# Kernel tuning notes

Hardware: AMD Instinct MI355X
Metric: run time of the kernel (lower is better)

Reference implementation:

```python
import jax, jax.numpy as jnp
import numpy as np

B, S, D, N, L, V = 2, 512, 1024, 4096, 4, 32000
EPS = 1e-5

def ternarize(w):
    # BitNet b1.58-style: scale = mean |w|, quantize to {-1,0,1}, rescale.
    s = jnp.mean(jnp.abs(w)) + 1e-8
    return s * jnp.round(jnp.clip(w / s, -1.0, 1.0))

def tern_ste(w):
    # straight-through estimator (faithful to ternary training)
    return w + jax.lax.stop_gradient(ternarize(w) - w)

def layer_norm(x, g, b):
    mu = jnp.mean(x, axis=-1, keepdims=True)
    var = jnp.var(x, axis=-1, keepdims=True)
    return (x - mu) * jax.lax.rsqrt(var + EPS) * g + b

def setup_inputs() -> dict:
    key = jax.random.key(0)
    ks = jax.random.split(key, 20)
    sc = lambda d: 1.0 / np.sqrt(d)
    inp = {
        'input_ids': jax.random.randint(ks[0], (B, S), 0, V, dtype=jnp.int32),
        'emb':       jax.random.normal(ks[1], (V, D), jnp.float32) * 0.02,
        'pos_emb':   jax.random.normal(ks[2], (S, D), jnp.float32) * 0.02,
        'gru_wih':   jax.random.normal(ks[3], (3 * D, D), jnp.float32) * sc(D),
        'gru_whh':   jax.random.normal(ks[4], (3 * D, D), jnp.float32) * sc(D),
        'gru_bih':   jnp.zeros((3 * D,), jnp.float32),
        'gru_bhh':   jnp.zeros((3 * D,), jnp.float32),
        'syn_w':     jax.random.normal(ks[5], (L, N, D), jnp.float32) * sc(D),
        'syn_b':     jnp.zeros((L, N), jnp.float32),
        'out_w':     jax.random.normal(ks[6], (L, D, N), jnp.float32) * sc(N),
        'out_b':     jnp.zeros((L, D), jnp.float32),
        'ln_g':      jnp.ones((L, D), jnp.float32),
        'ln_b':      jnp.zeros((L, D), jnp.float32),
        'on_g':      jnp.ones((D,), jnp.float32),
        'on_b':      jnp.zeros((D,), jnp.float32),
        'head_w':    jax.random.normal(ks[7], (V, D), jnp.float32) * sc(D),
        'head_b':    jnp.zeros((V,), jnp.float32),
    }
    return inp

def gru(x, wih, whh, bih, bhh):
    # x: [B,S,D] -> [B,S,D], torch nn.GRU semantics, h0 = 0
    # Precompute input projections for all timesteps: [B,S,3D]
    gi_all = jnp.einsum('bsd,ed->bse', x, wih) + bih
    def step(h, gi):
        gh = h @ whh.T + bhh
        ir, iz, inn = jnp.split(gi, 3, axis=-1)
        hr, hz, hn = jnp.split(gh, 3, axis=-1)
        r = jax.nn.sigmoid(ir + hr)
        z = jax.nn.sigmoid(iz + hz)
        n = jnp.tanh(inn + r * hn)
        h_new = (1.0 - z) * n + z * h
        return h_new, h_new
    h0 = jnp.zeros((x.shape[0], whh.shape[1]), x.dtype)
    _, hs = jax.lax.scan(step, h0, jnp.swapaxes(gi_all, 0, 1))
    return jnp.swapaxes(hs, 0, 1)

def reference(input_ids, emb, pos_emb, gru_wih, gru_whh, gru_bih, gru_bhh,
              syn_w, syn_b, out_w, out_b, ln_g, ln_b, on_g, on_b,
              head_w, head_b):
    # Ternary embedding lookup
    x = tern_ste(emb)[input_ids]                       # [B,S,D]
    x = x + pos_emb[None, :x.shape[1], :]
    x = gru(x, gru_wih, gru_whh, gru_bih, gru_bhh)
    for l in range(L):
        residual = x
        hidden = jax.nn.relu(jnp.einsum('bsd,nd->bsn', x, tern_ste(syn_w[l])) + syn_b[l])
        out = jnp.einsum('bsn,dn->bsd', hidden, tern_ste(out_w[l])) + out_b[l]
        x = layer_norm(residual + out, ln_g[l], ln_b[l])
    x = layer_norm(x, on_g, on_b)
    logits = jnp.einsum('bsd,vd->bsv', x, tern_ste(head_w)) + head_b  # [B,S,V]
    return logits
```

## Files before the change

### kernel.cpp

```cpp
#include <hip/hip_runtime.h>
#include <hip/hip_bf16.h>
#include <cstdint>
#include <cstddef>

#define Dm 1024
#define Sm 512
#define Bm 2
#define Nm 4096
#define Lm 4
#define Vm 32000

typedef __attribute__((ext_vector_type(8))) short short8;
typedef __attribute__((ext_vector_type(4))) float floatx4;

struct PrepArgs {
  const float* src[9];
  unsigned short* dst[9];
  long n4[9];
  int sidx[9];
  int njobs;
};

__device__ __forceinline__ unsigned short f2b(float f){
  union { float f; unsigned u; } v; v.f = f;
  unsigned r = (v.u + 0x7fffu + ((v.u >> 16) & 1u)) >> 16;
  return (unsigned short)r;
}
__device__ __forceinline__ float b2f(unsigned short h){
  union { unsigned u; float f; } v; v.u = ((unsigned)h) << 16;
  return v.f;
}

__device__ __forceinline__ void gload16(const unsigned short* g, unsigned short* l){
  __builtin_amdgcn_global_load_lds(
      (const __attribute__((address_space(1))) void*)g,
      (__attribute__((address_space(3))) void*)l, 16, 0, 0);
}

__global__ __launch_bounds__(256) void absum_all_kernel(
    const float* __restrict__ emb, const float* __restrict__ syn_w,
    const float* __restrict__ out_w, const float* __restrict__ head_w,
    double* __restrict__ partial)
{
  int wid = blockIdx.x >> 7;
  int blk = blockIdx.x & 127;
  const float* base; long n4;
  if (wid == 0){ base = emb; n4 = (long)Vm * Dm / 4; }
  else if (wid <= 4){ base = syn_w + (size_t)(wid - 1) * Nm * Dm; n4 = (long)Nm * Dm / 4; }
  else if (wid <= 8){ base = out_w + (size_t)(wid - 5) * Dm * Nm; n4 = (long)Nm * Dm / 4; }
  else { base = head_w; n4 = (long)Vm * Dm / 4; }

  long i = (long)blk * 256 + threadIdx.x;
  const long stride = 128L * 256;
  double s = 0.0;
  for (; i < n4; i += stride){
    float4 v = ((const float4*)base)[i];
    s += (double)fabsf(v.x) + (double)fabsf(v.y) + (double)fabsf(v.z) + (double)fabsf(v.w);
  }
  #pragma unroll
  for (int off = 32; off; off >>= 1) s += __shfl_down(s, off, 64);
  __shared__ double wsum[4];
  int lane = threadIdx.x & 63, wv = threadIdx.x >> 6;
  if (lane == 0) wsum[wv] = s;
  __syncthreads();
  if (threadIdx.x == 0) partial[wid * 128 + blk] = wsum[0] + wsum[1] + wsum[2] + wsum[3];
}

__global__ __launch_bounds__(128) void scale_kernel(const double* __restrict__ partials,
                                                    float* __restrict__ scales){
  int b = blockIdx.x;
  int tid = threadIdx.x;
  __shared__ double red[128];
  red[tid] = partials[b * 128 + tid];
  __syncthreads();
  for (int off = 64; off; off >>= 1){
    if (tid < off) red[tid] += red[tid + off];
    __syncthreads();
  }
  if (tid == 0){
    double cnt = (b == 0 || b == 9) ? (double)Vm * (double)Dm : (double)Nm * (double)Dm;
    scales[b] = (float)(red[0] / cnt);
  }
}

__global__ __launch_bounds__(256) void tern_kernel(const float* __restrict__ w,
                                                   const float* __restrict__ smean,
                                                   unsigned short* __restrict__ out, long n4){
  float s = smean[0] + 1e-8f;
  long i = (long)blockIdx.x * blockDim.x + threadIdx.x;
  long stride = (long)gridDim.x * blockDim.x;
  for (; i < n4; i += stride){
    float4 v = ((const float4*)w)[i];
    ushort4 o;
    o.x = f2b(rintf(fminf(fmaxf(v.x / s, -1.f), 1.f)));
    o.y = f2b(rintf(fminf(fmaxf(v.y / s, -1.f), 1.f)));
    o.z = f2b(rintf(fminf(fmaxf(v.z / s, -1.f), 1.f)));
    o.w = f2b(rintf(fminf(fmaxf(v.w / s, -1.f), 1.f)));
    ((ushort4*)out)[i] = o;
  }
}

__global__ __launch_bounds__(256) void embed_split_kernel(
    const int* __restrict__ ids, const float* __restrict__ emb,
    const float* __restrict__ pos, const float* __restrict__ smean,
    unsigned short* __restrict__ xhi, unsigned short* __restrict__ xlo,
    const float* __restrict__ wih, unsigned short* __restrict__ whi,
    unsigned short* __restrict__ wlo)
{
  if (blockIdx.x < 1024){
    int row = blockIdx.x;
    int sp  = row & (Sm - 1);
    int id  = ids[row];
    float s = smean[0] + 1e-8f;
    int d = threadIdx.x * 4;
    float4 wv = *(const float4*)(emb + (size_t)id * Dm + d);
    float4 pv = *(const float4*)(pos + (size_t)sp * Dm + d);
    float y[4];
    y[0] = s * rintf(fminf(fmaxf(wv.x / s, -1.f), 1.f)) + pv.x;
    y[1] = s * rintf(fminf(fmaxf(wv.y / s, -1.f), 1.f)) + pv.y;
    y[2] = s * rintf(fminf(fmaxf(wv.z / s, -1.f), 1.f)) + pv.z;
    y[3] = s * rintf(fminf(fmaxf(wv.w / s, -1.f), 1.f)) + pv.w;
    ushort4 h4, l4;
    unsigned short* hp = (unsigned short*)&h4;
    unsigned short* lp = (unsigned short*)&l4;
    #pragma unroll
    for (int e = 0; e < 4; e++){
      unsigned short h = f2b(y[e]);
      hp[e] = h;
      lp[e] = f2b(y[e] - b2f(h));
    }
    size_t base = (size_t)row * Dm + d;
    *(ushort4*)(xhi + base) = h4;
    *(ushort4*)(xlo + base) = l4;
  } else {
    long i = (long)(blockIdx.x - 1024) * 256 + threadIdx.x;
    const long stride = 1024L * 256;
    const long n4 = (long)(3 * Dm) * Dm / 4;
    for (; i < n4; i += stride){
      float4 v = ((const float4*)wih)[i];
      float f[4] = {v.x, v.y, v.z, v.w};
      ushort4 h4, l4;
      unsigned short* hp = (unsigned short*)&h4;
      unsigned short* lp = (unsigned short*)&l4;
      #pragma unroll
      for (int e = 0; e < 4; e++){
        unsigned short h = f2b(f[e]);
        hp[e] = h;
        lp[e] = f2b(f[e] - b2f(h));
      }
      ((ushort4*)whi)[i] = h4;
      ((ushort4*)wlo)[i] = l4;
    }
  }
}

template<bool WSPLIT, bool WF32, int BT>
__global__ __launch_bounds__(256) void gemm_kernel(
    const unsigned short* __restrict__ Ahi, const unsigned short* __restrict__ Alo,
    const void* __restrict__ Wsrc, const unsigned short* __restrict__ Wlo,
    const float* __restrict__ bias, const float* __restrict__ smean,
    int relu, float* __restrict__ outf,
    unsigned short* __restrict__ outhi, unsigned short* __restrict__ outlo,
    int M, int N, int K)
{
  constexpr int WT = BT / 2;
  constexpr int FT = WT / 16;
  constexpr int RPT = 256 / BT;
  constexpr int CPT = 32 / RPT;
  constexpr int NU  = CPT / 8;

  __shared__ unsigned short As[2][BT][40];
  __shared__ unsigned short Bs[WSPLIT ? 2 : 1][BT][40];
  int tid = threadIdx.x;
  int wave = tid >> 6, lane = tid & 63;
  int wm = wave >> 1, wn = wave & 1;
  int bm = blockIdx.y, bn = blockIdx.x;

  bool tern = (smean != nullptr);
  float s = 1.f;
  if (tern) s = smean[0] + 1e-8f;

  int arow = tid / RPT, sub = tid % RPT;
  int col0 = sub * CPT;
  const unsigned short* Agh = Ahi + (size_t)(bm * BT + arow) * K + col0;
  const unsigned short* Agl = Alo + (size_t)(bm * BT + arow) * K + col0;
  const float* Wgf = nullptr;
  const unsigned short* Wgh = nullptr;
  const unsigned short* Wgl = nullptr;
  if (WF32) Wgf = (const float*)Wsrc + (size_t)(bn * BT + arow) * K + col0;
  else {
    Wgh = (const unsigned short*)Wsrc + (size_t)(bn * BT + arow) * K + col0;
    if (WSPLIT) Wgl = Wlo + (size_t)(bn * BT + arow) * K + col0;
  }

  floatx4 acc[FT][FT];
  #pragma unroll
  for (int i = 0; i < FT; i++)
    #pragma unroll
    for (int j = 0; j < FT; j++)
      acc[i][j] = (floatx4){0.f, 0.f, 0.f, 0.f};

  int kpb = K / (int)gridDim.z;
  int k_beg = blockIdx.z * kpb;

  for (int k0 = k_beg; k0 < k_beg + kpb; k0 += 32){
    __syncthreads();
    #pragma unroll
    for (int u = 0; u < NU; u++){
      *(uint4*)&As[0][arow][col0 + u * 8] = *(const uint4*)(Agh + k0 + u * 8);
      *(uint4*)&As[1][arow][col0 + u * 8] = *(const uint4*)(Agl + k0 + u * 8);
    }
    if (WF32){
      unsigned short tmp[CPT];
      #pragma unroll
      for (int q = 0; q < CPT / 4; q++){
        float4 wv = *(const float4*)(Wgf + k0 + q * 4);
        float f[4] = {wv.x, wv.y, wv.z, wv.w};
        #pragma unroll
        for (int e = 0; e < 4; e++){
          float w = f[e];
          if (tern) w = rintf(fminf(fmaxf(w / s, -1.f), 1.f));
          tmp[q * 4 + e] = f2b(w);
        }
      }
      #pragma unroll
      for (int u = 0; u < NU; u++)
        *(uint4*)&Bs[0][arow][col0 + u * 8] = *(uint4*)&tmp[u * 8];
    } else {
      #pragma unroll
      for (int u = 0; u < NU; u++){
        *(uint4*)&Bs[0][arow][col0 + u * 8] = *(const uint4*)(Wgh + k0 + u * 8);
        if (WSPLIT)
          *(uint4*)&Bs[1][arow][col0 + u * 8] = *(const uint4*)(Wgl + k0 + u * 8);
      }
    }
    __syncthreads();

    int kq = lane >> 4, mr = lane & 15;
    short8 afh[FT], afl[FT], bfh[FT];
    #pragma unroll
    for (int i = 0; i < FT; i++){
      afh[i] = *(const short8*)&As[0][wm*WT + i*16 + mr][kq*8];
      afl[i] = *(const short8*)&As[1][wm*WT + i*16 + mr][kq*8];
    }
    #pragma unroll
    for (int j = 0; j < FT; j++) bfh[j] = *(const short8*)&Bs[0][wn*WT + j*16 + mr][kq*8];
    #pragma unroll
    for (int i = 0; i < FT; i++)
      #pragma unroll
      for (int j = 0; j < FT; j++){
        acc[i][j] = __builtin_amdgcn_mfma_f32_16x16x32_bf16(afh[i], bfh[j], acc[i][j], 0, 0, 0);
        acc[i][j] = __builtin_amdgcn_mfma_f32_16x16x32_bf16(afl[i], bfh[j], acc[i][j], 0, 0, 0);
      }
    if (WSPLIT){
      short8 bfl[FT];
      #pragma unroll
      for (int j = 0; j < FT; j++) bfl[j] = *(const short8*)&Bs[1][wn*WT + j*16 + mr][kq*8];
      #pragma unroll
      for (int i = 0; i < FT; i++)
        #pragma unroll
        for (int j = 0; j < FT; j++)
          acc[i][j] = __builtin_amdgcn_mfma_f32_16x16x32_bf16(afh[i], bfl[j], acc[i][j], 0, 0, 0);
    }
  }

  bool split = (gridDim.z > 1);
  bool addb = (blockIdx.z == 0);
  int cr = lane >> 4, cc = lane & 15;
  #pragma unroll
  for (int j = 0; j < FT; j++){
    int col = bn * BT + wn * WT + j * 16 + cc;
    float bv = (bias && addb) ? bias[col] : 0.f;
    #pragma unroll
    for (int i = 0; i < FT; i++){
      #pragma unroll
      for (int r = 0; r < 4; r++){
        int row = bm * BT + wm * WT + i * 16 + cr * 4 + r;
        float v = acc[i][j][r] * s + bv;
        if (relu) v = fmaxf(v, 0.f);
        size_t idx = (size_t)row * N + col;
        if (outf){
          if (split) atomicAdd(outf + idx, v);
          else outf[idx] = v;
        }
        if (outhi){
          unsigned short h = f2b(v);
          outhi[idx] = h;
          outlo[idx] = f2b(v - b2f(h));
        }
      }
    }
  }
}

__global__ __launch_bounds__(256) void gemm_lds_kernel(
    const unsigned short* __restrict__ Ahi, const unsigned short* __restrict__ Alo,
    const unsigned short* __restrict__ Whi,
    const float* __restrict__ bias, const float* __restrict__ smean,
    int relu, float* __restrict__ outf, int M, int N, int K)
{
  int nbm = M / 128, nbn = N / 128;
  int id = blockIdx.x;
  int xcd = id & 7;
  int sblk = id >> 3;
  int bm = sblk % nbm;
  int q = sblk / nbm;
  int bn = xcd + 8 * q;
  if (bn >= nbn) return;

  __shared__ __align__(16) unsigned short lds[3 * 4096];
  int tid = threadIdx.x;
  int wave = tid >> 6, lane = tid & 63;
  int wm = wave >> 1, wn = wave & 1;

  float s = 1.f;
  if (smean) s = smean[0] + 1e-8f;

  int r0 = wave * 32 + (lane >> 2);
  int r1 = r0 + 16;
  int s0 = (lane & 3) ^ ((r0 >> 1) & 3);
  int s1 = (lane & 3) ^ ((r1 >> 1) & 3);
  const unsigned short* ga0 = Ahi + (size_t)(bm * 128 + r0) * K + s0 * 8;
  const unsigned short* ga1 = Ahi + (size_t)(bm * 128 + r1) * K + s1 * 8;
  const unsigned short* gl0 = Alo + (size_t)(bm * 128 + r0) * K + s0 * 8;
  const unsigned short* gl1 = Alo + (size_t)(bm * 128 + r1) * K + s1 * 8;
  const unsigned short* gw0 = Whi + (size_t)(bn * 128 + r0) * K + s0 * 8;
  const unsigned short* gw1 = Whi + (size_t)(bn * 128 + r1) * K + s1 * 8;
  unsigned short* la = &lds[wave * 1024];

  floatx4 acc[4][4];
  #pragma unroll
  for (int i = 0; i < 4; i++)
    #pragma unroll
    for (int j = 0; j < 4; j++)
      acc[i][j] = (floatx4){0.f, 0.f, 0.f, 0.f};

  for (int k0 = 0; k0 < K; k0 += 32){
    __syncthreads();
    gload16(ga0 + k0, la);
    gload16(ga1 + k0, la + 512);
    gload16(gl0 + k0, la + 4096);
    gload16(gl1 + k0, la + 4096 + 512);
    gload16(gw0 + k0, la + 8192);
    gload16(gw1 + k0, la + 8192 + 512);
    __syncthreads();

    int kq = lane >> 4, mr = lane & 15;
    short8 afh[4], afl[4], bfh[4];
    #pragma unroll
    for (int i = 0; i < 4; i++){
      int r = wm * 64 + i * 16 + mr;
      int off = r * 32 + ((kq ^ ((r >> 1) & 3)) << 3);
      afh[i] = *(const short8*)&lds[off];
      afl[i] = *(const short8*)&lds[4096 + off];
    }
    #pragma unroll
    for (int j = 0; j < 4; j++){
      int r = wn * 64 + j * 16 + mr;
      int off = r * 32 + ((kq ^ ((r >> 1) & 3)) << 3);
      bfh[j] = *(const short8*)&lds[8192 + off];
    }
    #pragma unroll
    for (int i = 0; i < 4; i++)
      #pragma unroll
      for (int j = 0; j < 4; j++){
        acc[i][j] = __builtin_amdgcn_mfma_f32_16x16x32_bf16(afh[i], bfh[j], acc[i][j], 0, 0, 0);
        acc[i][j] = __builtin_amdgcn_mfma_f32_16x16x32_bf16(afl[i], bfh[j], acc[i][j], 0, 0, 0);
      }
  }

  int cr = lane >> 4, cc = lane & 15;
  #pragma unroll
  for (int j = 0; j < 4; j++){
    int col = bn * 128 + wn * 64 + j * 16 + cc;
    float bv = bias ? bias[col] : 0.f;
    #pragma unroll
    for (int i = 0; i < 4; i++){
      #pragma unroll
      for (int r = 0; r < 4; r++){
        int row = bm * 128 + wm * 64 + i * 16 + cr * 4 + r;
        float v = acc[i][j][r] * s + bv;
        if (relu) v = fmaxf(v, 0.f);
        outf[(size_t)row * N + col] = v;
      }
    }
  }
}

#define NGRU 64
__global__ __launch_bounds__(1024) void gru_kernel(
    const float* __restrict__ gi, const float* __restrict__ whh, const float* __restrict__ bhh,
    unsigned long long* __restrict__ hbuf, float* __restrict__ hs,
    unsigned short* __restrict__ xhi, unsigned short* __restrict__ xlo,
    const float* __restrict__ scales, PrepArgs pa)
{
  if (blockIdx.x >= NGRU){
    long pid = blockIdx.x - NGRU;
    long stride = (long)(gridDim.x - NGRU) * 1024;
    for (int j = 0; j < pa.njobs; j++){
      float s = scales[pa.sidx[j]] + 1e-8f;
      const float4* s4 = (const float4*)pa.src[j];
      ushort4* d4 = (ushort4*)pa.dst[j];
      long n4 = pa.n4[j];
      for (long k = pid * 1024 + threadIdx.x; k < n4; k += stride){
        float4 v = s4[k];
        ushort4 o;
        o.x = f2b(rintf(fminf(fmaxf(v.x / s, -1.f), 1.f)));
        o.y = f2b(rintf(fminf(fmaxf(v.y / s, -1.f), 1.f)));
        o.z = f2b(rintf(fminf(fmaxf(v.z / s, -1.f), 1.f)));
        o.w = f2b(rintf(fminf(fmaxf(v.w / s, -1.f), 1.f)));
        d4[k] = o;
      }
    }
    return;
  }

  __shared__ float lds_h[2 * 1088];
  __shared__ float lds_gh[96];
  int w = blockIdx.x, tid = threadIdx.x;
  int d0 = w * 16;
  int o = tid >> 4, c = tid & 15;
  bool active = (o < 48);
  int g = o >> 4, dl = o & 15;
  int wrow = g * Dm + d0 + dl;
  float wreg[64];
  if (active){
    const float* src = whh + (size_t)wrow * Dm + c * 64;
    #pragma unroll
    for (int i = 0; i < 64; i++) wreg[i] = src[i];
  }
  float bhval = active ? bhh[wrow] : 0.f;

  int bb = tid >> 4, dd = tid & 15;
  float hprev = 0.f;

  for (int t = 0; t < Sm; t++){
    float ir = 0.f, iz = 0.f, inn = 0.f;
    if (tid < 32){
      const float* girow = gi + ((size_t)bb * Sm + t) * (3 * Dm);
      int d = d0 + dd;
      ir  = girow[d];
      iz  = girow[Dm + d];
      inn = girow[2 * Dm + d];
    }
    {
      const unsigned long long* src = hbuf + (size_t)(t & 1) * 2048 + tid * 2;
      unsigned got = 0;
      int spins = 0;
      while (got != 3u){
        #pragma unroll
        for (int q = 0; q < 2; q++){
          if (!(got & (1u << q))){
            unsigned long long wd = __hip_atomic_load(src + q, __ATOMIC_RELAXED,
                                                      __HIP_MEMORY_SCOPE_AGENT);
            if ((unsigned)(wd >> 32) == (unsigned)t){
              union { unsigned u; float f; } cv; cv.u = (unsigned)wd;
              int wi = tid * 2 + q;
              int b = wi >> 10, d = wi & 1023;
              lds_h[b * 1088 + (d >> 6) * 68 + (d & 63)] = cv.f;
              got |= 1u << q;
            }
          }
        }
        if (got != 3u){
          if (++spins > (1 << 20)) break;
          __builtin_amdgcn_s_sleep(1);
        }
      }
    }
    __syncthreads();
    if (active){
      const float* hp = lds_h + c * 68;
      float a0 = 0.f, a1 = 0.f;
      #pragma unroll
      for (int q = 0; q < 16; q++){
        float4 h0 = *(const float4*)(hp + q * 4);
        float4 h1 = *(const float4*)(hp + 1088 + q * 4);
        a0 += wreg[q*4+0] * h0.x; a1 += wreg[q*4+0] * h1.x;
        a0 += wreg[q*4+1] * h0.y; a1 += wreg[q*4+1] * h1.y;
        a0 += wreg[q*4+2] * h0.z; a1 += wreg[q*4+2] * h1.z;
        a0 += wreg[q*4+3] * h0.w; a1 += wreg[q*4+3] * h1.w;
      }
      #pragma unroll
      for (int off = 8; off; off >>= 1){
        a0 += __shfl_xor(a0, off, 16);
        a1 += __shfl_xor(a1, off, 16);
      }
      if (c == 0){
        lds_gh[o]      = a0 + bhval;
        lds_gh[48 + o] = a1 + bhval;
      }
    }
    __syncthreads();
    if (tid < 32){
      float gr = lds_gh[bb * 48 + dd];
      float gz = lds_gh[bb * 48 + 16 + dd];
      float gn = lds_gh[bb * 48 + 32 + dd];
      float rr = 1.f / (1.f + expf(-(ir + gr)));
      float zz = 1.f / (1.f + expf(-(iz + gz)));
      float nn = tanhf(inn + rr * gn);
      float hnew = (1.f - zz) * nn + zz * hprev;
      hprev = hnew;
      int d = d0 + dd;
      union { float f; unsigned u; } cv; cv.f = hnew;
      unsigned long long wd = ((unsigned long long)(unsigned)(t + 1) << 32) | (unsigned long long)cv.u;
      __hip_atomic_store(hbuf + (size_t)((t + 1) & 1) * 2048 + bb * Dm + d, wd,
                         __ATOMIC_RELAXED, __HIP_MEMORY_SCOPE_AGENT);
      size_t oi = ((size_t)bb * Sm + t) * Dm + d;
      hs[oi] = hnew;
      unsigned short h = f2b(hnew);
      xhi[oi] = h;
      xlo[oi] = f2b(hnew - b2f(h));
    }
  }
}

__global__ __launch_bounds__(256) void ln_kernel(
    const float* __restrict__ resid, const float* __restrict__ addv,
    const float* __restrict__ g, const float* __restrict__ b,
    float* __restrict__ outf, unsigned short* __restrict__ outhi,
    unsigned short* __restrict__ outlo)
{
  int row = blockIdx.x;
  int d = threadIdx.x * 4;
  size_t base = (size_t)row * Dm + d;
  float4 v = *(const float4*)(resid + base);
  if (addv){
    float4 a = *(const float4*)(addv + base);
    v.x += a.x; v.y += a.y; v.z += a.z; v.w += a.w;
  }
  float sum = v.x + v.y + v.z + v.w;
  float sq  = v.x*v.x + v.y*v.y + v.z*v.z + v.w*v.w;
  #pragma unroll
  for (int off = 32; off; off >>= 1){
    sum += __shfl_down(sum, off, 64);
    sq  += __shfl_down(sq,  off, 64);
  }
  __shared__ float red[4][2];
  __shared__ float bc[2];
  int lane = threadIdx.x & 63, wv = threadIdx.x >> 6;
  if (lane == 0){ red[wv][0] = sum; red[wv][1] = sq; }
  __syncthreads();
  if (threadIdx.x == 0){
    float st = red[0][0] + red[1][0] + red[2][0] + red[3][0];
    float qt = red[0][1] + red[1][1] + red[2][1] + red[3][1];
    float mu = st * (1.f / Dm);
    float var = qt * (1.f / Dm) - mu * mu;
    bc[0] = mu; bc[1] = rsqrtf(var + 1e-5f);
  }
  __syncthreads();
  float mu = bc[0], rs = bc[1];
  float4 gv = *(const float4*)(g + d);
  float4 bv = *(const float4*)(b + d);
  float y[4];
  y[0] = (v.x - mu) * rs * gv.x + bv.x;
  y[1] = (v.y - mu) * rs * gv.y + bv.y;
  y[2] = (v.z - mu) * rs * gv.z + bv.z;
  y[3] = (v.w - mu) * rs * gv.w + bv.w;
  if (outf) *(float4*)(outf + base) = *(float4*)y;
  if (outhi){
    ushort4 h4, l4;
    unsigned short* hp = (unsigned short*)&h4;
    unsigned short* lp = (unsigned short*)&l4;
    #pragma unroll
    for (int e = 0; e < 4; e++){
      unsigned short h = f2b(y[e]);
      hp[e] = h;
      lp[e] = f2b(y[e] - b2f(h));
    }
    *(ushort4*)(outhi + base) = h4;
    *(ushort4*)(outlo + base) = l4;
  }
}

extern "C" void kernel_launch(void* const* d_in, const int* in_sizes, int n_in,
                              void* d_out, int out_size, void* d_ws, size_t ws_size,
                              hipStream_t stream)
{
  const int*   ids    = (const int*)  d_in[0];
  const float* emb    = (const float*)d_in[1];
  const float* pos    = (const float*)d_in[2];
  const float* wih    = (const float*)d_in[3];
  const float* whh    = (const float*)d_in[4];
  const float* bih    = (const float*)d_in[5];
  const float* bhh    = (const float*)d_in[6];
  const float* syn_w  = (const float*)d_in[7];
  const float* syn_b  = (const float*)d_in[8];
  const float* out_w  = (const float*)d_in[9];
  const float* out_b  = (const float*)d_in[10];
  const float* ln_g   = (const float*)d_in[11];
  const float* ln_b   = (const float*)d_in[12];
  const float* on_g   = (const float*)d_in[13];
  const float* on_b   = (const float*)d_in[14];
  const float* head_w = (const float*)d_in[15];
  const float* head_b = (const float*)d_in[16];
  float* logits = (float*)d_out;

  const size_t MB = (size_t)1 << 20;
  char* ws = (char*)d_ws;
  float*  scales   = (float*) ws;
  double* partials = (double*)(ws + 32768);
  unsigned long long* hbuf = (unsigned long long*)(ws + 131072);
  float*          hs     = (float*)         (ws + 1  * MB);
  unsigned short* xhi    = (unsigned short*)(ws + 5  * MB);
  unsigned short* xlo    = (unsigned short*)(ws + 7  * MB);
  float*          outbuf = (float*)         (ws + 9  * MB);
  float*          gi     = (float*)         (ws + 13 * MB);
  unsigned short* ltbuf  = (unsigned short*)(ws + 13 * MB);
  unsigned short* wih_hi = (unsigned short*)(ws + 25 * MB);
  unsigned short* wih_lo = (unsigned short*)(ws + 31 * MB);
  unsigned short* hhi    = (unsigned short*)(ws + 37 * MB);
  unsigned short* hlo    = (unsigned short*)(ws + 45 * MB);
  unsigned short* wbuf   = (unsigned short*)(ws + 53 * MB);

  bool pre_layer = ws_size >= 62  * MB;
  bool pre_head  = ws_size >= 120 * MB;
  bool tier1     = ws_size >= 192 * MB;

  PrepArgs pa; pa.njobs = 0;
  unsigned short* synp[Lm] = {nullptr, nullptr, nullptr, nullptr};
  unsigned short* outp[Lm] = {nullptr, nullptr, nullptr, nullptr};
  auto addjob = [&](const float* s, unsigned short* d, long n4, int si){
    pa.src[pa.njobs] = s; pa.dst[pa.njobs] = d; pa.n4[pa.njobs] = n4; pa.sidx[pa.njobs] = si;
    pa.njobs++;
  };
  if (pre_head){
    addjob(head_w, wbuf, (long)Vm * Dm / 4, 9);
    if (tier1){
      for (int l = 0; l < Lm; l++){
        synp[l] = (unsigned short*)(ws + 120 * MB + (size_t)l * 8 * MB);
        outp[l] = (unsigned short*)(ws + 152 * MB + (size_t)l * 8 * MB);
        addjob(syn_w + (size_t)l * Nm * Dm, synp[l], (long)Nm * Dm / 4, 1 + l);
        addjob(out_w + (size_t)l * Dm * Nm, outp[l], (long)Nm * Dm / 4, 5 + l);
      }
    } else {
      synp[0] = (unsigned short*)(ws + 25 * MB);
      addjob(syn_w, synp[0], (long)Nm * Dm / 4, 1);
    }
  }

  hipMemsetAsync(d_ws, 0, 163840, stream);

  absum_all_kernel<<<1280, 256, 0, stream>>>(emb, syn_w, out_w, head_w, partials);
  scale_kernel<<<10, 128, 0, stream>>>(partials, scales);

  embed_split_kernel<<<2048, 256, 0, stream>>>(ids, emb, pos, scales, xhi, xlo,
                                               wih, wih_hi, wih_lo);

  gemm_kernel<true, false, 64><<<dim3(3072/64, 1024/64, 1), 256, 0, stream>>>(
      xhi, xlo, wih_hi, wih_lo, bih, nullptr, 0, gi, nullptr, nullptr, 1024, 3072, 1024);

  gru_kernel<<<NGRU + 192, 1024, 0, stream>>>(gi, whh, bhh, hbuf, hs, xhi, xlo, scales, pa);

  for (int l = 0; l < Lm; l++){
    if (pre_head){
      unsigned short* sw = synp[l];
      if (!sw){
        tern_kernel<<<2048, 256, 0, stream>>>(syn_w + (size_t)l * Nm * Dm, scales + 1 + l,
                                              ltbuf, (long)Nm * Dm / 4);
        sw = ltbuf;
      }
      gemm_kernel<false, false, 64><<<dim3(4096/64, 1024/64, 1), 256, 0, stream>>>(
          xhi, xlo, sw, nullptr, syn_b + (size_t)l * Nm, scales + 1 + l,
          1, nullptr, hhi, hlo, 1024, 4096, 1024);
      hipMemsetAsync(outbuf, 0, (size_t)1024 * 1024 * 4, stream);
      unsigned short* ow = outp[l];
      if (!ow){
        tern_kernel<<<2048, 256, 0, stream>>>(out_w + (size_t)l * Dm * Nm, scales + 5 + l,
                                              ltbuf, (long)Dm * Nm / 4);
        ow = ltbuf;
      }
      gemm_kernel<false, false, 64><<<dim3(1024/64, 1024/64, 2), 256, 0, stream>>>(
          hhi, hlo, ow, nullptr, out_b + (size_t)l * Dm, scales + 5 + l,
          0, outbuf, nullptr, nullptr, 1024, 1024, 4096);
    } else if (pre_layer){
      tern_kernel<<<2048, 256, 0, stream>>>(syn_w + (size_t)l * Nm * Dm, scales + 1 + l,
                                            wbuf, (long)Nm * Dm / 4);
      gemm_kernel<false, false, 64><<<dim3(4096/64, 1024/64, 1), 256, 0, stream>>>(
          xhi, xlo, wbuf, nullptr, syn_b + (size_t)l * Nm, scales + 1 + l,
          1, nullptr, hhi, hlo, 1024, 4096, 1024);
      hipMemsetAsync(outbuf, 0, (size_t)1024 * 1024 * 4, stream);
      tern_kernel<<<2048, 256, 0, stream>>>(out_w + (size_t)l * Dm * Nm, scales + 5 + l,
                                            wbuf, (long)Dm * Nm / 4);
      gemm_kernel<false, false, 64><<<dim3(1024/64, 1024/64, 2), 256, 0, stream>>>(
          hhi, hlo, wbuf, nullptr, out_b + (size_t)l * Dm, scales + 5 + l,
          0, outbuf, nullptr, nullptr, 1024, 1024, 4096);
    } else {
      gemm_kernel<false, true, 64><<<dim3(4096/64, 1024/64, 1), 256, 0, stream>>>(
          xhi, xlo, syn_w + (size_t)l * Nm * Dm, nullptr, syn_b + (size_t)l * Nm, scales + 1 + l,
          1, nullptr, hhi, hlo, 1024, 4096, 1024);
      hipMemsetAsync(outbuf, 0, (size_t)1024 * 1024 * 4, stream);
      gemm_kernel<false, true, 64><<<dim3(1024/64, 1024/64, 2), 256, 0, stream>>>(
          hhi, hlo, out_w + (size_t)l * Dm * Nm, nullptr, out_b + (size_t)l * Dm, scales + 5 + l,
          0, outbuf, nullptr, nullptr, 1024, 1024, 4096);
    }
    ln_kernel<<<1024, 256, 0, stream>>>(hs, outbuf, ln_g + (size_t)l * Dm, ln_b + (size_t)l * Dm,
                                        hs, xhi, xlo);
  }
  ln_kernel<<<1024, 256, 0, stream>>>(hs, nullptr, on_g, on_b, nullptr, xhi, xlo);

  if (pre_head){
    gemm_lds_kernel<<<2048, 256, 0, stream>>>(
        xhi, xlo, wbuf, head_b, scales + 9, 0, logits, 1024, 32000, 1024);
  } else {
    gemm_kernel<false, true, 128><<<dim3(32000/128, 1024/128, 1), 256, 0, stream>>>(
        xhi, xlo, head_w, nullptr, head_b, scales + 9, 0, logits, nullptr, nullptr, 1024, 32000, 1024);
  }
}
```

Before: 2.132 ms.

## Fold split-K output zeroing into GRU side blocks and layernorm kernel

Removes the per-layer hipMemsetAsync of the split-K output buffer on the tier1 path. The first buffer is zeroed by the GRU kernel's spare prep blocks, and later buffers are zeroed by extra blocks in the preceding layernorm launch, ping-ponging between two buffers. The prep blocks also sleep briefly before starting, likely to let the GRU blocks get scheduled first. This saves several memset launches at the cost of extra blocks, a sleep delay, and reusing the gi region as a second buffer.

```diff
diff --git a/kernel.cpp b/kernel.cpp
--- a/kernel.cpp
+++ b/kernel.cpp
@@ -14,10 +14,10 @@
 typedef __attribute__((ext_vector_type(4))) float floatx4;
 
 struct PrepArgs {
-  const float* src[9];
-  unsigned short* dst[9];
-  long n4[9];
-  int sidx[9];
+  const float* src[10];
+  unsigned short* dst[10];
+  long n4[10];
+  int sidx[10];
   int njobs;
 };
 
@@ -395,21 +395,30 @@
     const float* __restrict__ scales, PrepArgs pa)
 {
   if (blockIdx.x >= NGRU){
+    if (pa.njobs > 0){
+      for (int i = 0; i < 20; i++) __builtin_amdgcn_s_sleep(127);
+    }
     long pid = blockIdx.x - NGRU;
     long stride = (long)(gridDim.x - NGRU) * 1024;
     for (int j = 0; j < pa.njobs; j++){
-      float s = scales[pa.sidx[j]] + 1e-8f;
       const float4* s4 = (const float4*)pa.src[j];
       ushort4* d4 = (ushort4*)pa.dst[j];
       long n4 = pa.n4[j];
-      for (long k = pid * 1024 + threadIdx.x; k < n4; k += stride){
-        float4 v = s4[k];
-        ushort4 o;
-        o.x = f2b(rintf(fminf(fmaxf(v.x / s, -1.f), 1.f)));
-        o.y = f2b(rintf(fminf(fmaxf(v.y / s, -1.f), 1.f)));
-        o.z = f2b(rintf(fminf(fmaxf(v.z / s, -1.f), 1.f)));
-        o.w = f2b(rintf(fminf(fmaxf(v.w / s, -1.f), 1.f)));
-        d4[k] = o;
+      if (s4){
+        float s = scales[pa.sidx[j]] + 1e-8f;
+        for (long k = pid * 1024 + threadIdx.x; k < n4; k += stride){
+          float4 v = s4[k];
+          ushort4 o;
+          o.x = f2b(rintf(fminf(fmaxf(v.x / s, -1.f), 1.f)));
+          o.y = f2b(rintf(fminf(fmaxf(v.y / s, -1.f), 1.f)));
+          o.z = f2b(rintf(fminf(fmaxf(v.z / s, -1.f), 1.f)));
+          o.w = f2b(rintf(fminf(fmaxf(v.w / s, -1.f), 1.f)));
+          d4[k] = o;
+        }
+      } else {
+        ushort4 z = make_ushort4(0, 0, 0, 0);
+        for (long k = pid * 1024 + threadIdx.x; k < n4; k += stride)
+          d4[k] = z;
       }
     }
     return;
@@ -519,8 +528,18 @@
     const float* __restrict__ resid, const float* __restrict__ addv,
     const float* __restrict__ g, const float* __restrict__ b,
     float* __restrict__ outf, unsigned short* __restrict__ outhi,
-    unsigned short* __restrict__ outlo)
+    unsigned short* __restrict__ outlo, float* __restrict__ zbuf)
 {
+  if (blockIdx.x >= 1024){
+    if (zbuf){
+      long i = (long)(blockIdx.x - 1024) * 256 + threadIdx.x;
+      float4 z = {0.f, 0.f, 0.f, 0.f};
+      #pragma unroll
+      for (int q = 0; q < 4; q++)
+        ((float4*)zbuf)[i + (long)q * 65536] = z;
+    }
+    return;
+  }
   int row = blockIdx.x;
   int d = threadIdx.x * 4;
   size_t base = (size_t)row * Dm + d;
@@ -604,8 +623,9 @@
   float*          hs     = (float*)         (ws + 1  * MB);
   unsigned short* xhi    = (unsigned short*)(ws + 5  * MB);
   unsigned short* xlo    = (unsigned short*)(ws + 7  * MB);
-  float*          outbuf = (float*)         (ws + 9  * MB);
+  float*          outbufA = (float*)        (ws + 9  * MB);
   float*          gi     = (float*)         (ws + 13 * MB);
+  float*          outbufB = (float*)        (ws + 13 * MB);
   unsigned short* ltbuf  = (unsigned short*)(ws + 13 * MB);
   unsigned short* wih_hi = (unsigned short*)(ws + 25 * MB);
   unsigned short* wih_lo = (unsigned short*)(ws + 31 * MB);
@@ -633,6 +653,7 @@
         addjob(syn_w + (size_t)l * Nm * Dm, synp[l], (long)Nm * Dm / 4, 1 + l);
         addjob(out_w + (size_t)l * Dm * Nm, outp[l], (long)Nm * Dm / 4, 5 + l);
       }
+      addjob(nullptr, (unsigned short*)outbufA, (long)4 * MB / 8, 0);
     } else {
       synp[0] = (unsigned short*)(ws + 25 * MB);
       addjob(syn_w, synp[0], (long)Nm * Dm / 4, 1);
@@ -653,6 +674,8 @@
   gru_kernel<<<NGRU + 192, 1024, 0, stream>>>(gi, whh, bhh, hbuf, hs, xhi, xlo, scales, pa);
 
   for (int l = 0; l < Lm; l++){
+    float* ob      = (tier1 && (l & 1)) ? outbufB : outbufA;
+    float* ob_next = (tier1 && !((l + 1) & 1)) ? outbufA : outbufB;
     if (pre_head){
       unsigned short* sw = synp[l];
       if (!sw){
@@ -663,7 +686,7 @@
       gemm_kernel<false, false, 64><<<dim3(4096/64, 1024/64, 1), 256, 0, stream>>>(
           xhi, xlo, sw, nullptr, syn_b + (size_t)l * Nm, scales + 1 + l,
           1, nullptr, hhi, hlo, 1024, 4096, 1024);
-      hipMemsetAsync(outbuf, 0, (size_t)1024 * 1024 * 4, stream);
+      if (!tier1) hipMemsetAsync(ob, 0, (size_t)1024 * 1024 * 4, stream);
       unsigned short* ow = outp[l];
       if (!ow){
         tern_kernel<<<2048, 256, 0, stream>>>(out_w + (size_t)l * Dm * Nm, scales + 5 + l,
@@ -672,32 +695,33 @@
       }
       gemm_kernel<false, false, 64><<<dim3(1024/64, 1024/64, 2), 256, 0, stream>>>(
           hhi, hlo, ow, nullptr, out_b + (size_t)l * Dm, scales + 5 + l,
-          0, outbuf, nullptr, nullptr, 1024, 1024, 4096);
+          0, ob, nullptr, nullptr, 1024, 1024, 4096);
     } else if (pre_layer){
       tern_kernel<<<2048, 256, 0, stream>>>(syn_w + (size_t)l * Nm * Dm, scales + 1 + l,
                                             wbuf, (long)Nm * Dm / 4);
       gemm_kernel<false, false, 64><<<dim3(4096/64, 1024/64, 1), 256, 0, stream>>>(
           xhi, xlo, wbuf, nullptr, syn_b + (size_t)l * Nm, scales + 1 + l,
           1, nullptr, hhi, hlo, 1024, 4096, 1024);
-      hipMemsetAsync(outbuf, 0, (size_t)1024 * 1024 * 4, stream);
+      hipMemsetAsync(ob, 0, (size_t)1024 * 1024 * 4, stream);
       tern_kernel<<<2048, 256, 0, stream>>>(out_w + (size_t)l * Dm * Nm, scales + 5 + l,
                                             wbuf, (long)Dm * Nm / 4);
       gemm_kernel<false, false, 64><<<dim3(1024/64, 1024/64, 2), 256, 0, stream>>>(
           hhi, hlo, wbuf, nullptr, out_b + (size_t)l * Dm, scales + 5 + l,
-          0, outbuf, nullptr, nullptr, 1024, 1024, 4096);
+          0, ob, nullptr, nullptr, 1024, 1024, 4096);
     } else {
       gemm_kernel<false, true, 64><<<dim3(4096/64, 1024/64, 1), 256, 0, stream>>>(
           xhi, xlo, syn_w + (size_t)l * Nm * Dm, nullptr, syn_b + (size_t)l * Nm, scales + 1 + l,
           1, nullptr, hhi, hlo, 1024, 4096, 1024);
-      hipMemsetAsync(outbuf, 0, (size_t)1024 * 1024 * 4, stream);
+      hipMemsetAsync(ob, 0, (size_t)1024 * 1024 * 4, stream);
       gemm_kernel<false, true, 64><<<dim3(1024/64, 1024/64, 2), 256, 0, stream>>>(
           hhi, hlo, out_w + (size_t)l * Dm * Nm, nullptr, out_b + (size_t)l * Dm, scales + 5 + l,
-          0, outbuf, nullptr, nullptr, 1024, 1024, 4096);
-    }
-    ln_kernel<<<1024, 256, 0, stream>>>(hs, outbuf, ln_g + (size_t)l * Dm, ln_b + (size_t)l * Dm,
-                                        hs, xhi, xlo);
-  }
-  ln_kernel<<<1024, 256, 0, stream>>>(hs, nullptr, on_g, on_b, nullptr, xhi, xlo);
+          0, ob, nullptr, nullptr, 1024, 1024, 4096);
+    }
+    float* zb = (tier1 && l < Lm - 1) ? ob_next : nullptr;
+    ln_kernel<<<zb ? 1280 : 1024, 256, 0, stream>>>(
+        hs, ob, ln_g + (size_t)l * Dm, ln_b + (size_t)l * Dm, hs, xhi, xlo, zb);
+  }
+  ln_kernel<<<1024, 256, 0, stream>>>(hs, nullptr, on_g, on_b, nullptr, xhi, xlo, nullptr);
 
   if (pre_head){
     gemm_lds_kernel<<<2048, 256, 0, stream>>>(
```

Measured after the change: 2.130 ms (median of 2 runs). No clear change (-0.1%).
